# Optimization experiments

Hardware: AMD Instinct MI355X
Metric: run time of the kernel (lower is better)

Reference implementation:

```python
import jax, jax.numpy as jnp
import numpy as np


def lstm_encode(x, Wih, Whh, b):
    """x: [S, T, F] -> final hidden state [S, H]. PyTorch LSTM gate order (i, f, g, o)."""
    S = x.shape[0]
    H = Whh.shape[1]

    def step(carry, xt):
        h, c = carry
        z = xt @ Wih.T + h @ Whh.T + b  # [S, 4H]
        i, f, g, o = jnp.split(z, 4, axis=-1)
        c = jax.nn.sigmoid(f) * c + jax.nn.sigmoid(i) * jnp.tanh(g)
        h = jax.nn.sigmoid(o) * jnp.tanh(c)
        return (h, c), None

    init = (jnp.zeros((S, H), x.dtype), jnp.zeros((S, H), x.dtype))
    (h, _), _ = jax.lax.scan(step, init, jnp.swapaxes(x, 0, 1))
    return h


def gatv2(h, Ws, Wd, a, bias):
    """Dense GATv2 on batched fully-connected graphs (no self loops).
    h: [G, N, Hin]; Ws, Wd: [nh, Hin, O]; a: [nh, O]; bias: [nh, O] -> [G, N, nh, O].
    Graph is fully connected (all i != j), so edge-softmax == dense row softmax
    with the diagonal masked out; this is the efficient dense form of the
    gather / LeakyReLU / edge-softmax / scatter pattern in DGL's GATv2Conv."""
    nh = Ws.shape[0]
    N = h.shape[1]
    self_mask = jnp.eye(N, dtype=bool)
    outs = []
    for hd in range(nh):  # small fixed head count; loop caps peak memory
        fs = h @ Ws[hd]  # [G, N, O] source-projected feats (messages)
        fd = h @ Wd[hd]  # [G, N, O] dst-projected feats
        e = jax.nn.leaky_relu(fd[:, :, None, :] + fs[:, None, :, :], 0.2)  # [G, dst, src, O]
        logits = jnp.where(self_mask, -jnp.inf, e @ a[hd])  # [G, dst, src]
        attn = jax.nn.softmax(logits, axis=-1)
        outs.append(jnp.einsum('gds,gso->gdo', attn, fs) + bias[hd])
    return jnp.stack(outs, axis=2)


def cosine(x, y, eps=1e-6):
    xn = x / jnp.maximum(jnp.linalg.norm(x, axis=-1, keepdims=True), eps)
    yn = y / jnp.maximum(jnp.linalg.norm(y, axis=-1, keepdims=True), eps)
    return (xn * yn).sum(-1)


def setup_inputs() -> dict:
    key = jax.random.key(0)
    B, K, T, N, F, H, GH, NH = 16, 4, 64, 128, 16, 32, 32, 8
    ks = jax.random.split(key, 16)

    def rn(k, shape, scale=1.0):
        return jax.random.normal(k, shape, jnp.float32) * scale

    return {
        'anchor': rn(ks[0], (B, T, N, F)),
        'pos': rn(ks[1], (B, T, N, F)),
        'neg': rn(ks[2], (B, K, T, N, F)),
        'hideout': rn(ks[3], (B, 2)),
        'timestep': jax.random.uniform(ks[4], (B, 1), jnp.float32),
        'Wih': rn(ks[5], (4 * H, F), 1.0 / np.sqrt(F)),
        'Whh': rn(ks[6], (4 * H, H), 1.0 / np.sqrt(H)),
        'b_lstm': rn(ks[7], (4 * H,), 0.1),
        'W1s': rn(ks[8], (NH, H, H), 1.0 / np.sqrt(H)),
        'W1d': rn(ks[9], (NH, H, H), 1.0 / np.sqrt(H)),
        'a1': rn(ks[10], (NH, H), 1.0 / np.sqrt(H)),
        'b1': rn(ks[11], (NH, H), 0.1),
        'W2s': rn(ks[12], (1, H, GH), 1.0 / np.sqrt(H)),
        'W2d': rn(ks[13], (1, H, GH), 1.0 / np.sqrt(H)),
        'a2': rn(ks[14], (1, GH), 1.0 / np.sqrt(GH)),
        'b2': rn(ks[15], (1, GH), 0.1),
        'num_agents': 128,
    }


def reference(anchor, pos, neg, hideout, timestep, Wih, Whh, b_lstm,
              W1s, W1d, a1, b1, W2s, W2d, a2, b2, num_agents):
    B, T, N, F = anchor.shape
    K = neg.shape[1]
    H = Whh.shape[1]
    # per-agent time series -> LSTM sequences
    a_seq = jnp.transpose(anchor, (0, 2, 1, 3)).reshape(B * N, T, F)
    p_seq = jnp.transpose(pos, (0, 2, 1, 3)).reshape(B * N, T, F)
    n_seq = jnp.transpose(neg, (0, 1, 3, 2, 4)).reshape(B * K * N, T, F)
    hn = lstm_encode(jnp.concatenate([a_seq, p_seq, n_seq], 0), Wih, Whh, b_lstm)
    hg = hn.reshape(-1, N, H)  # [(2+K)*B, N, H] batched fully-connected graphs
    h1 = gatv2(hg, W1s, W1d, a1, b1).mean(axis=2)  # mean over 8 heads
    h2 = gatv2(h1, W2s, W2d, a2, b2)[:, :, 0, :]   # single head, squeezed
    pooled = h2.mean(axis=1)                        # AvgPooling over nodes
    anchor_res = pooled[:B]
    pos_res = pooled[B:2 * B]
    neg_res = pooled[2 * B:].reshape(B, K, -1)
    sim_pos = cosine(anchor_res, pos_res)[:, None]      # [B, 1]
    sim_neg = cosine(anchor_res[:, None, :], neg_res)   # [B, K]
    all_vecs = jnp.concatenate([sim_neg, sim_pos], axis=1)  # positive last
    contrastive = (-jax.nn.log_softmax(all_vecs, axis=1)[:, -1]).mean()
    res = jnp.concatenate([anchor_res, hideout, timestep], axis=-1)
    return res, contrastive
```

## Files before the change

### kernel.cpp

```cpp
#include <hip/hip_runtime.h>
#include <math.h>


typedef __bf16 bf16x8 __attribute__((ext_vector_type(8)));
typedef float  f32x4  __attribute__((ext_vector_type(4)));
typedef unsigned int u32x4 __attribute__((ext_vector_type(4)));

__device__ __forceinline__ float fast_rcp(float x) { return __builtin_amdgcn_rcpf(x); }
__device__ __forceinline__ float sigm(float x)     { return fast_rcp(1.f + __expf(-x)); }
__device__ __forceinline__ float tanh_fast(float x){ return fmaf(2.f, fast_rcp(1.f + __expf(-2.f * x)), -1.f); }

#define KEEP4(x) asm volatile("" : "+v"(x))

__global__ __launch_bounds__(256, 1) void lstm_mfma_kernel(
    const float* __restrict__ anchor, const float* __restrict__ pos,
    const float* __restrict__ neg, const float* __restrict__ Wih,
    const float* __restrict__ Whh, const float* __restrict__ bias,
    float* __restrict__ hn)
{
    __shared__ unsigned int Hbuf[4][512];
    const int tid  = threadIdx.x;
    const int w    = tid >> 6;
    const int lane = tid & 63;
    const int l15  = lane & 15;
    const int g4   = lane >> 4;
    unsigned int* hb = Hbuf[w];

    #pragma unroll
    for (int i = 0; i < 8; ++i) hb[lane + i * 64] = 0u;

    u32x4 whhH[8], whhL[8], wihH[8];
    float bq[8];
    #pragma unroll
    for (int f = 0; f < 8; ++f) {
        const int G = f >> 1, Hh = f & 1;
        const int c = G * 32 + Hh * 16 + l15;
        bq[f] = bias[c];
        union { u32x4 u; bf16x8 v; } th, tl, ti;
        const float* wr = Whh + c * 32 + g4 * 8;
        #pragma unroll
        for (int i = 0; i < 8; ++i) {
            float wv = wr[i];
            __bf16 hi = (__bf16)wv;
            th.v[i] = hi;
            tl.v[i] = (__bf16)(wv - (float)hi);
        }
        if (g4 < 2) {
            const float* wr2 = Wih + c * 16 + g4 * 8;
            #pragma unroll
            for (int i = 0; i < 8; ++i) ti.v[i] = (__bf16)wr2[i];
        } else {
            #pragma unroll
            for (int i = 0; i < 8; ++i) ti.v[i] = (__bf16)0.f;
        }
        whhH[f] = th.u; whhL[f] = tl.u; wihH[f] = ti.u;
    }
    #pragma unroll
    for (int f = 0; f < 8; ++f) { KEEP4(whhH[f]); KEEP4(whhL[f]); KEEP4(wihH[f]); }

    const int s = blockIdx.x * 64 + w * 16 + l15;
    const float* xbase; int sl;
    if (s < 2048)      { xbase = anchor; sl = s; }
    else if (s < 4096) { xbase = pos;    sl = s - 2048; }
    else               { xbase = neg;    sl = s - 4096; }
    const bool xact = (g4 < 2);
    const float* xp = xbase + (sl >> 7) * 131072 + (sl & 127) * 16 + (xact ? g4 * 8 : 0);

    const float4 z4 = make_float4(0.f, 0.f, 0.f, 0.f);
    float4 xaA = z4, xbA = z4, xaB = z4, xbB = z4;
    if (xact) {
        xaA = *(const float4*)(xp);        xbA = *(const float4*)(xp + 4);
        xaB = *(const float4*)(xp + 2048); xbB = *(const float4*)(xp + 2052);
    }

    float cst[8] = {0.f,0.f,0.f,0.f,0.f,0.f,0.f,0.f};
    float hv[8]  = {0.f,0.f,0.f,0.f,0.f,0.f,0.f,0.f};

    #define LSTM_STEP(XA, XB)                                                          \
    {                                                                                  \
        bf16x8 ax;                                                                     \
        ax[0]=(__bf16)XA.x; ax[1]=(__bf16)XA.y; ax[2]=(__bf16)XA.z; ax[3]=(__bf16)XA.w;\
        ax[4]=(__bf16)XB.x; ax[5]=(__bf16)XB.y; ax[6]=(__bf16)XB.z; ax[7]=(__bf16)XB.w;\
        const int c0 = g4 * 2;                                                         \
        const int swz = (l15 & 3) << 1;                                                \
        uint4 v0 = *(const uint4*)(hb + l15 * 32 + ((c0 ^ swz) << 2));                 \
        uint4 v1 = *(const uint4*)(hb + l15 * 32 + (((c0 + 1) ^ swz) << 2));           \
        union { unsigned int u[4]; bf16x8 v; } ahi, alo;                               \
        ahi.u[0] = __builtin_amdgcn_perm(v0.y, v0.x, 0x05040100u);                     \
        ahi.u[1] = __builtin_amdgcn_perm(v0.w, v0.z, 0x05040100u);                     \
        ahi.u[2] = __builtin_amdgcn_perm(v1.y, v1.x, 0x05040100u);                     \
        ahi.u[3] = __builtin_amdgcn_perm(v1.w, v1.z, 0x05040100u);                     \
        alo.u[0] = __builtin_amdgcn_perm(v0.y, v0.x, 0x07060302u);                     \
        alo.u[1] = __builtin_amdgcn_perm(v0.w, v0.z, 0x07060302u);                     \
        alo.u[2] = __builtin_amdgcn_perm(v1.y, v1.x, 0x07060302u);                     \
        alo.u[3] = __builtin_amdgcn_perm(v1.w, v1.z, 0x07060302u);                     \
        f32x4 z[8];                                                                    \
        _Pragma("unroll")                                                              \
        for (int f = 0; f < 8; ++f) {                                                  \
            f32x4 a = __builtin_amdgcn_mfma_f32_16x16x32_bf16(                         \
                ax, __builtin_bit_cast(bf16x8, wihH[f]), (f32x4)(0.f), 0, 0, 0);       \
            a = __builtin_amdgcn_mfma_f32_16x16x32_bf16(                               \
                ahi.v, __builtin_bit_cast(bf16x8, whhH[f]), a, 0, 0, 0);               \
            a = __builtin_amdgcn_mfma_f32_16x16x32_bf16(                               \
                ahi.v, __builtin_bit_cast(bf16x8, whhL[f]), a, 0, 0, 0);               \
            a = __builtin_amdgcn_mfma_f32_16x16x32_bf16(                               \
                alo.v, __builtin_bit_cast(bf16x8, whhH[f]), a, 0, 0, 0);               \
            z[f] = a;                                                                  \
        }                                                                              \
        _Pragma("unroll")                                                              \
        for (int Hh = 0; Hh < 2; ++Hh) {                                               \
            _Pragma("unroll")                                                          \
            for (int r = 0; r < 4; ++r) {                                              \
                const int idx = Hh * 4 + r;                                            \
                float zi = z[0 + Hh][r] + bq[0 + Hh];                                  \
                float zf = z[2 + Hh][r] + bq[2 + Hh];                                  \
                float zg = z[4 + Hh][r] + bq[4 + Hh];                                  \
                float zo = z[6 + Hh][r] + bq[6 + Hh];                                  \
                float cn = fmaf(sigm(zf), cst[idx], sigm(zi) * tanh_fast(zg));         \
                cst[idx] = cn;                                                         \
                float h = sigm(zo) * tanh_fast(cn);                                    \
                hv[idx] = h;                                                           \
                __bf16 hh_ = (__bf16)h;                                                \
                __bf16 hl_ = (__bf16)(h - (float)hh_);                                 \
                unsigned int pk = (unsigned int)__builtin_bit_cast(unsigned short, hh_)\
                                | ((unsigned int)__builtin_bit_cast(unsigned short, hl_) << 16); \
                const int mm = g4 * 4 + r;                                             \
                const int jw = Hh * 16 + l15;                                          \
                hb[mm * 32 + (((jw >> 2) ^ ((mm & 3) << 1)) << 2) + (jw & 3)] = pk;    \
            }                                                                          \
        }                                                                              \
    }

    for (int t = 0; t < 64; t += 2) {
        float4 cA1 = xaA, cA2 = xbA;
        if (xact && t + 2 < 64) {
            const float* p = xp + (t + 2) * 2048;
            xaA = *(const float4*)(p); xbA = *(const float4*)(p + 4);
        }
        LSTM_STEP(cA1, cA2);

        float4 cB1 = xaB, cB2 = xbB;
        if (xact && t + 3 < 64) {
            const float* p = xp + (t + 3) * 2048;
            xaB = *(const float4*)(p); xbB = *(const float4*)(p + 4);
        }
        LSTM_STEP(cB1, cB2);
    }
    #undef LSTM_STEP

    const int seq0 = blockIdx.x * 64 + w * 16;
    #pragma unroll
    for (int Hh = 0; Hh < 2; ++Hh) {
        #pragma unroll
        for (int r = 0; r < 4; ++r) {
            hn[(seq0 + g4 * 4 + r) * 32 + Hh * 16 + l15] = hv[Hh * 4 + r];
        }
    }
}

__global__ __launch_bounds__(256) void gat1_kernel(
    const float* __restrict__ hn, const float* __restrict__ W1s,
    const float* __restrict__ W1d, const float* __restrict__ a1,
    const float* __restrict__ b1, float* __restrict__ h1heads)
{
    const int g = blockIdx.x >> 3, hd = blockIdx.x & 7;
    __shared__ float FS[128][36];
    __shared__ float FD[128][36];
    __shared__ float AVr[32];
    __shared__ float As06[128];
    __shared__ float Ad06[128];
    const int tid = threadIdx.x;

    if (tid < 32) AVr[tid] = a1[hd * 32 + tid];

    {
        const int o = tid & 31, nb = tid >> 5;
        float wcs[32], wcd[32];
        const float* wsp = W1s + hd * 1024 + o;
        const float* wdp = W1d + hd * 1024 + o;
        #pragma unroll
        for (int k = 0; k < 32; ++k) { wcs[k] = wsp[k * 32]; wcd[k] = wdp[k * 32]; }
        const float* hp = hn + g * 4096 + nb * 512;
        #pragma unroll 1
        for (int n = 0; n < 16; ++n) {
            float a0 = 0.f, a1_ = 0.f, b0 = 0.f, b1_ = 0.f;
            #pragma unroll
            for (int k0 = 0; k0 < 32; k0 += 4) {
                float4 hv = *(const float4*)(hp + n * 32 + k0);
                a0 = fmaf(hv.x, wcs[k0+0], a0); b0 = fmaf(hv.x, wcd[k0+0], b0);
                a1_ = fmaf(hv.y, wcs[k0+1], a1_); b1_ = fmaf(hv.y, wcd[k0+1], b1_);
                a0 = fmaf(hv.z, wcs[k0+2], a0); b0 = fmaf(hv.z, wcd[k0+2], b0);
                a1_ = fmaf(hv.w, wcs[k0+3], a1_); b1_ = fmaf(hv.w, wcd[k0+3], b1_);
            }
            FS[nb * 16 + n][o] = a0 + a1_;
            FD[nb * 16 + n][o] = b0 + b1_;
        }
    }
    __syncthreads();

    if (tid < 128) {
        float ss = 0.f, sd = 0.f;
        #pragma unroll
        for (int oo = 0; oo < 32; ++oo) {
            int o = (oo + tid) & 31;
            float a = AVr[o];
            ss = fmaf(a, FS[tid][o], ss);
            sd = fmaf(a, FD[tid][o], sd);
        }
        As06[tid] = 0.6f * ss;
        Ad06[tid] = 0.6f * sd;
    }
    __syncthreads();

    const int d = tid >> 1, sbase = (tid & 1) << 6;
    float fdr[32], avs[32];
    #pragma unroll
    for (int c = 0; c < 8; ++c) {
        float4 v = *(const float4*)&FD[d][c * 4];
        fdr[c*4+0] = v.x; fdr[c*4+1] = v.y; fdr[c*4+2] = v.z; fdr[c*4+3] = v.w;
        float4 w = *(const float4*)&AVr[c * 4];
        avs[c*4+0] = 0.4f * w.x; avs[c*4+1] = 0.4f * w.y;
        avs[c*4+2] = 0.4f * w.z; avs[c*4+3] = 0.4f * w.w;
    }
    const float adc = Ad06[d];

    float Z = 0.f;
    float acc[32];
    #pragma unroll
    for (int o = 0; o < 32; ++o) acc[o] = 0.f;
    #pragma unroll 1
    for (int si = 0; si < 64; ++si) {
        const int s = sbase + si;
        float4 fa[8];
        #pragma unroll
        for (int c = 0; c < 8; ++c) fa[c] = *(const float4*)&FS[s][c * 4];
        float c0 = 0.f, c1 = 0.f, c2 = 0.f, c3 = 0.f;
        #pragma unroll
        for (int c = 0; c < 8; ++c) {
            float e0 = fdr[c*4+0] + fa[c].x; c0 = fmaf(avs[c*4+0], __builtin_fabsf(e0), c0);
            float e1 = fdr[c*4+1] + fa[c].y; c1 = fmaf(avs[c*4+1], __builtin_fabsf(e1), c1);
            float e2 = fdr[c*4+2] + fa[c].z; c2 = fmaf(avs[c*4+2], __builtin_fabsf(e2), c2);
            float e3 = fdr[c*4+3] + fa[c].w; c3 = fmaf(avs[c*4+3], __builtin_fabsf(e3), c3);
        }
        float v = adc + As06[s] + ((c0 + c1) + (c2 + c3));
        float e = (s == d) ? 0.f : __expf(v);
        Z += e;
        #pragma unroll
        for (int c = 0; c < 8; ++c) {
            acc[c*4+0] = fmaf(e, fa[c].x, acc[c*4+0]);
            acc[c*4+1] = fmaf(e, fa[c].y, acc[c*4+1]);
            acc[c*4+2] = fmaf(e, fa[c].z, acc[c*4+2]);
            acc[c*4+3] = fmaf(e, fa[c].w, acc[c*4+3]);
        }
    }
    Z += __shfl_xor(Z, 1);
    const float rz = fast_rcp(Z);
    #pragma unroll
    for (int o = 0; o < 32; ++o) acc[o] += __shfl_xor(acc[o], 1);

    float* dst = h1heads + ((size_t)((g * 8 + hd) * 128 + d)) * 32;
    const float* bp = b1 + hd * 32;
    if ((tid & 1) == 0) {
        #pragma unroll
        for (int c = 0; c < 4; ++c) {
            float4 v;
            v.x = fmaf(acc[c*4+0], rz, bp[c*4+0]);
            v.y = fmaf(acc[c*4+1], rz, bp[c*4+1]);
            v.z = fmaf(acc[c*4+2], rz, bp[c*4+2]);
            v.w = fmaf(acc[c*4+3], rz, bp[c*4+3]);
            *(float4*)(dst + c * 4) = v;
        }
    } else {
        #pragma unroll
        for (int c = 4; c < 8; ++c) {
            float4 v;
            v.x = fmaf(acc[c*4+0], rz, bp[c*4+0]);
            v.y = fmaf(acc[c*4+1], rz, bp[c*4+1]);
            v.z = fmaf(acc[c*4+2], rz, bp[c*4+2]);
            v.w = fmaf(acc[c*4+3], rz, bp[c*4+3]);
            *(float4*)(dst + c * 4) = v;
        }
    }
}

__global__ __launch_bounds__(256) void gat2_kernel(
    const float* __restrict__ h1heads, const float* __restrict__ W2s,
    const float* __restrict__ W2d, const float* __restrict__ a2,
    const float* __restrict__ b2, float* __restrict__ pooled)
{
    const int g = blockIdx.x;
    __shared__ float HS[128][36];
    __shared__ float FS[128][36];
    __shared__ float FD[128][36];
    __shared__ float AVr[32];
    __shared__ float As06[128];
    __shared__ float Ad06[128];
    const int tid = threadIdx.x;

    if (tid < 32) AVr[tid] = a2[tid];

    {
        #pragma unroll
        for (int i = 0; i < 4; ++i) {
            int idx4 = i * 256 + tid;
            float sx = 0.f, sy = 0.f, sz = 0.f, sw = 0.f;
            #pragma unroll
            for (int hdd = 0; hdd < 8; ++hdd) {
                const float4* src = (const float4*)(h1heads + (size_t)(g * 8 + hdd) * 4096);
                float4 v = src[idx4];
                sx += v.x; sy += v.y; sz += v.z; sw += v.w;
            }
            int n = idx4 >> 3, k0 = (idx4 & 7) * 4;
            float4 r; r.x = sx * 0.125f; r.y = sy * 0.125f; r.z = sz * 0.125f; r.w = sw * 0.125f;
            *(float4*)&HS[n][k0] = r;
        }
    }
    __syncthreads();

    {
        const int o = tid & 31, nb = tid >> 5;
        float wcs[32], wcd[32];
        const float* wsp = W2s + o;
        const float* wdp = W2d + o;
        #pragma unroll
        for (int k = 0; k < 32; ++k) { wcs[k] = wsp[k * 32]; wcd[k] = wdp[k * 32]; }
        #pragma unroll 1
        for (int n = nb * 16; n < nb * 16 + 16; ++n) {
            float a0 = 0.f, a1_ = 0.f, b0 = 0.f, b1_ = 0.f;
            #pragma unroll
            for (int k0 = 0; k0 < 32; k0 += 4) {
                const float4 hv = *(const float4*)&HS[n][k0];
                a0 = fmaf(hv.x, wcs[k0+0], a0); b0 = fmaf(hv.x, wcd[k0+0], b0);
                a1_ = fmaf(hv.y, wcs[k0+1], a1_); b1_ = fmaf(hv.y, wcd[k0+1], b1_);
                a0 = fmaf(hv.z, wcs[k0+2], a0); b0 = fmaf(hv.z, wcd[k0+2], b0);
                a1_ = fmaf(hv.w, wcs[k0+3], a1_); b1_ = fmaf(hv.w, wcd[k0+3], b1_);
            }
            FS[n][o] = a0 + a1_;
            FD[n][o] = b0 + b1_;
        }
    }
    __syncthreads();

    if (tid < 128) {
        float ss = 0.f, sd = 0.f;
        #pragma unroll
        for (int oo = 0; oo < 32; ++oo) {
            int o = (oo + tid) & 31;
            float a = AVr[o];
            ss = fmaf(a, FS[tid][o], ss);
            sd = fmaf(a, FD[tid][o], sd);
        }
        As06[tid] = 0.6f * ss;
        Ad06[tid] = 0.6f * sd;
    }
    __syncthreads();

    const int d = tid >> 1, sbase = (tid & 1) << 6;
    float fdr[32], avs[32];
    #pragma unroll
    for (int c = 0; c < 8; ++c) {
        float4 v = *(const float4*)&FD[d][c * 4];
        fdr[c*4+0] = v.x; fdr[c*4+1] = v.y; fdr[c*4+2] = v.z; fdr[c*4+3] = v.w;
        float4 w = *(const float4*)&AVr[c * 4];
        avs[c*4+0] = 0.4f * w.x; avs[c*4+1] = 0.4f * w.y;
        avs[c*4+2] = 0.4f * w.z; avs[c*4+3] = 0.4f * w.w;
    }
    const float adc = Ad06[d];

    float Z = 0.f;
    float acc[32];
    #pragma unroll
    for (int o = 0; o < 32; ++o) acc[o] = 0.f;
    #pragma unroll 1
    for (int si = 0; si < 64; ++si) {
        const int s = sbase + si;
        float4 fa[8];
        #pragma unroll
        for (int c = 0; c < 8; ++c) fa[c] = *(const float4*)&FS[s][c * 4];
        float c0 = 0.f, c1 = 0.f, c2 = 0.f, c3 = 0.f;
        #pragma unroll
        for (int c = 0; c < 8; ++c) {
            float e0 = fdr[c*4+0] + fa[c].x; c0 = fmaf(avs[c*4+0], __builtin_fabsf(e0), c0);
            float e1 = fdr[c*4+1] + fa[c].y; c1 = fmaf(avs[c*4+1], __builtin_fabsf(e1), c1);
            float e2 = fdr[c*4+2] + fa[c].z; c2 = fmaf(avs[c*4+2], __builtin_fabsf(e2), c2);
            float e3 = fdr[c*4+3] + fa[c].w; c3 = fmaf(avs[c*4+3], __builtin_fabsf(e3), c3);
        }
        float v = adc + As06[s] + ((c0 + c1) + (c2 + c3));
        float e = (s == d) ? 0.f : __expf(v);
        Z += e;
        #pragma unroll
        for (int c = 0; c < 8; ++c) {
            acc[c*4+0] = fmaf(e, fa[c].x, acc[c*4+0]);
            acc[c*4+1] = fmaf(e, fa[c].y, acc[c*4+1]);
            acc[c*4+2] = fmaf(e, fa[c].z, acc[c*4+2]);
            acc[c*4+3] = fmaf(e, fa[c].w, acc[c*4+3]);
        }
    }
    Z += __shfl_xor(Z, 1);
    const float rz = fast_rcp(Z);
    #pragma unroll
    for (int o = 0; o < 32; ++o) acc[o] += __shfl_xor(acc[o], 1);

    __syncthreads();
    if ((tid & 1) == 0) {
        #pragma unroll
        for (int c = 0; c < 4; ++c) {
            float4 v;
            v.x = acc[c*4+0] * rz; v.y = acc[c*4+1] * rz;
            v.z = acc[c*4+2] * rz; v.w = acc[c*4+3] * rz;
            *(float4*)&FD[d][c * 4] = v;
        }
    } else {
        #pragma unroll
        for (int c = 4; c < 8; ++c) {
            float4 v;
            v.x = acc[c*4+0] * rz; v.y = acc[c*4+1] * rz;
            v.z = acc[c*4+2] * rz; v.w = acc[c*4+3] * rz;
            *(float4*)&FD[d][c * 4] = v;
        }
    }
    __syncthreads();

    if (tid < 32) {
        float sp = 0.f;
        #pragma unroll 1
        for (int n = 0; n < 128; ++n) sp += FD[n][tid];
        pooled[g * 32 + tid] = fmaf(sp, 1.f / 128.f, b2[tid]);
    }
}

__global__ void final_kernel(const float* __restrict__ pooled,
                             const float* __restrict__ hideout,
                             const float* __restrict__ timestep,
                             float* __restrict__ out)
{
    const int b = threadIdx.x;
    __shared__ float lossArr[16];
    if (b < 16) {
        const float* A  = pooled + b * 32;
        const float* Pv = pooled + (16 + b) * 32;
        float av[32];
        float na = 0.f;
        #pragma unroll
        for (int i = 0; i < 32; ++i) { av[i] = A[i]; na += av[i] * av[i]; }
        float npv = 0.f, dp = 0.f;
        #pragma unroll
        for (int i = 0; i < 32; ++i) { float p = Pv[i]; npv += p * p; dp += av[i] * p; }
        const float eps = 1e-6f;
        const float ia = 1.f / fmaxf(sqrtf(na), eps);
        const float sp = dp * ia / fmaxf(sqrtf(npv), eps);
        float sn[4];
        #pragma unroll
        for (int k = 0; k < 4; ++k) {
            const float* Nv = pooled + (32 + b * 4 + k) * 32;
            float nn = 0.f, dn = 0.f;
            #pragma unroll
            for (int i = 0; i < 32; ++i) { float q = Nv[i]; nn += q * q; dn += av[i] * q; }
            sn[k] = dn * ia / fmaxf(sqrtf(nn), eps);
        }
        float m = sp;
        #pragma unroll
        for (int k = 0; k < 4; ++k) m = fmaxf(m, sn[k]);
        float Z = expf(sp - m);
        #pragma unroll
        for (int k = 0; k < 4; ++k) Z += expf(sn[k] - m);
        lossArr[b] = logf(Z) + m - sp;
        float* r = out + b * 35;
        #pragma unroll
        for (int i = 0; i < 32; ++i) r[i] = av[i];
        r[32] = hideout[b * 2];
        r[33] = hideout[b * 2 + 1];
        r[34] = timestep[b];
    }
    __syncthreads();
    if (b == 0) {
        float s = 0.f;
        #pragma unroll
        for (int i = 0; i < 16; ++i) s += lossArr[i];
        out[560] = s * (1.f / 16.f);
    }
}

extern "C" void kernel_launch(void* const* d_in, const int* in_sizes, int n_in,
                              void* d_out, int out_size, void* d_ws, size_t ws_size,
                              hipStream_t stream) {
    const float* anchor   = (const float*)d_in[0];
    const float* pos      = (const float*)d_in[1];
    const float* neg      = (const float*)d_in[2];
    const float* hideout  = (const float*)d_in[3];
    const float* timestep = (const float*)d_in[4];
    const float* Wih      = (const float*)d_in[5];
    const float* Whh      = (const float*)d_in[6];
    const float* b_lstm   = (const float*)d_in[7];
    const float* W1s      = (const float*)d_in[8];
    const float* W1d      = (const float*)d_in[9];
    const float* a1       = (const float*)d_in[10];
    const float* b1       = (const float*)d_in[11];
    const float* W2s      = (const float*)d_in[12];
    const float* W2d      = (const float*)d_in[13];
    const float* a2       = (const float*)d_in[14];
    const float* b2       = (const float*)d_in[15];
    float* out = (float*)d_out;

    char* ws = (char*)d_ws;
    float* hn      = (float*)(ws);
    float* h1heads = (float*)(ws + 1605632);
    float* pooled  = (float*)(ws + 14188544);

    hipLaunchKernelGGL(lstm_mfma_kernel, dim3(192), dim3(256), 0, stream,
                       anchor, pos, neg, Wih, Whh, b_lstm, hn);
    hipLaunchKernelGGL(gat1_kernel,  dim3(768),  dim3(256), 0, stream,
                       hn, W1s, W1d, a1, b1, h1heads);
    hipLaunchKernelGGL(gat2_kernel,  dim3(96),   dim3(256), 0, stream,
                       h1heads, W2s, W2d, a2, b2, pooled);
    hipLaunchKernelGGL(final_kernel, dim3(1),    dim3(64),  0, stream,
                       pooled, hideout, timestep, out);
}
```

Before: 177.7 us.

## Interleave two independent LSTM sequence tiles per wave and pad GAT FS rows

The LSTM kernel now has each wave process two 16-sequence tiles (A and B) together, interleaving their MFMA chains and activations. This hides the serial latency of the recurrent dependency chain, and the grid is halved from 192 to 96 blocks. In the GAT kernels the FS shared buffer gets an extra padding offset every 64 rows, so the two half-waves reading different source ranges land on different LDS banks. The cost is fewer blocks than the chip has compute units and higher register pressure in the LSTM kernel.

```diff
diff --git a/kernel.cpp b/kernel.cpp
--- a/kernel.cpp
+++ b/kernel.cpp
@@ -18,16 +18,17 @@
     const float* __restrict__ Whh, const float* __restrict__ bias,
     float* __restrict__ hn)
 {
-    __shared__ unsigned int Hbuf[4][512];
+    __shared__ unsigned int Hbuf[4][1024];
     const int tid  = threadIdx.x;
     const int w    = tid >> 6;
     const int lane = tid & 63;
     const int l15  = lane & 15;
     const int g4   = lane >> 4;
-    unsigned int* hb = Hbuf[w];
-
-    #pragma unroll
-    for (int i = 0; i < 8; ++i) hb[lane + i * 64] = 0u;
+    unsigned int* hbA = Hbuf[w];
+    unsigned int* hbB = Hbuf[w] + 512;
+
+    #pragma unroll
+    for (int i = 0; i < 16; ++i) Hbuf[w][lane + i * 64] = 0u;
 
     u32x4 whhH[8], whhL[8], wihH[8];
     float bq[8];
@@ -58,105 +59,152 @@
     #pragma unroll
     for (int f = 0; f < 8; ++f) { KEEP4(whhH[f]); KEEP4(whhL[f]); KEEP4(wihH[f]); }
 
-    const int s = blockIdx.x * 64 + w * 16 + l15;
-    const float* xbase; int sl;
-    if (s < 2048)      { xbase = anchor; sl = s; }
-    else if (s < 4096) { xbase = pos;    sl = s - 2048; }
-    else               { xbase = neg;    sl = s - 4096; }
     const bool xact = (g4 < 2);
-    const float* xp = xbase + (sl >> 7) * 131072 + (sl & 127) * 16 + (xact ? g4 * 8 : 0);
+    const float* xpA; const float* xpB;
+    {
+        const int sA = blockIdx.x * 128 + w * 32 + l15;
+        const int sB = sA + 16;
+        const float* base; int sl;
+        if (sA < 2048)      { base = anchor; sl = sA; }
+        else if (sA < 4096) { base = pos;    sl = sA - 2048; }
+        else                { base = neg;    sl = sA - 4096; }
+        xpA = base + (sl >> 7) * 131072 + (sl & 127) * 16 + (xact ? g4 * 8 : 0);
+        if (sB < 2048)      { base = anchor; sl = sB; }
+        else if (sB < 4096) { base = pos;    sl = sB - 2048; }
+        else                { base = neg;    sl = sB - 4096; }
+        xpB = base + (sl >> 7) * 131072 + (sl & 127) * 16 + (xact ? g4 * 8 : 0);
+    }
 
     const float4 z4 = make_float4(0.f, 0.f, 0.f, 0.f);
-    float4 xaA = z4, xbA = z4, xaB = z4, xbB = z4;
+    float4 eA0 = z4, eA1 = z4, oA0 = z4, oA1 = z4;
+    float4 eB0 = z4, eB1 = z4, oB0 = z4, oB1 = z4;
     if (xact) {
-        xaA = *(const float4*)(xp);        xbA = *(const float4*)(xp + 4);
-        xaB = *(const float4*)(xp + 2048); xbB = *(const float4*)(xp + 2052);
-    }
-
-    float cst[8] = {0.f,0.f,0.f,0.f,0.f,0.f,0.f,0.f};
-    float hv[8]  = {0.f,0.f,0.f,0.f,0.f,0.f,0.f,0.f};
-
-    #define LSTM_STEP(XA, XB)                                                          \
-    {                                                                                  \
-        bf16x8 ax;                                                                     \
-        ax[0]=(__bf16)XA.x; ax[1]=(__bf16)XA.y; ax[2]=(__bf16)XA.z; ax[3]=(__bf16)XA.w;\
-        ax[4]=(__bf16)XB.x; ax[5]=(__bf16)XB.y; ax[6]=(__bf16)XB.z; ax[7]=(__bf16)XB.w;\
-        const int c0 = g4 * 2;                                                         \
-        const int swz = (l15 & 3) << 1;                                                \
-        uint4 v0 = *(const uint4*)(hb + l15 * 32 + ((c0 ^ swz) << 2));                 \
-        uint4 v1 = *(const uint4*)(hb + l15 * 32 + (((c0 + 1) ^ swz) << 2));           \
-        union { unsigned int u[4]; bf16x8 v; } ahi, alo;                               \
-        ahi.u[0] = __builtin_amdgcn_perm(v0.y, v0.x, 0x05040100u);                     \
-        ahi.u[1] = __builtin_amdgcn_perm(v0.w, v0.z, 0x05040100u);                     \
-        ahi.u[2] = __builtin_amdgcn_perm(v1.y, v1.x, 0x05040100u);                     \
-        ahi.u[3] = __builtin_amdgcn_perm(v1.w, v1.z, 0x05040100u);                     \
-        alo.u[0] = __builtin_amdgcn_perm(v0.y, v0.x, 0x07060302u);                     \
-        alo.u[1] = __builtin_amdgcn_perm(v0.w, v0.z, 0x07060302u);                     \
-        alo.u[2] = __builtin_amdgcn_perm(v1.y, v1.x, 0x07060302u);                     \
-        alo.u[3] = __builtin_amdgcn_perm(v1.w, v1.z, 0x07060302u);                     \
-        f32x4 z[8];                                                                    \
-        _Pragma("unroll")                                                              \
-        for (int f = 0; f < 8; ++f) {                                                  \
-            f32x4 a = __builtin_amdgcn_mfma_f32_16x16x32_bf16(                         \
-                ax, __builtin_bit_cast(bf16x8, wihH[f]), (f32x4)(0.f), 0, 0, 0);       \
-            a = __builtin_amdgcn_mfma_f32_16x16x32_bf16(                               \
-                ahi.v, __builtin_bit_cast(bf16x8, whhH[f]), a, 0, 0, 0);               \
-            a = __builtin_amdgcn_mfma_f32_16x16x32_bf16(                               \
-                ahi.v, __builtin_bit_cast(bf16x8, whhL[f]), a, 0, 0, 0);               \
-            a = __builtin_amdgcn_mfma_f32_16x16x32_bf16(                               \
-                alo.v, __builtin_bit_cast(bf16x8, whhH[f]), a, 0, 0, 0);               \
-            z[f] = a;                                                                  \
-        }                                                                              \
+        eA0 = *(const float4*)(xpA);        eA1 = *(const float4*)(xpA + 4);
+        oA0 = *(const float4*)(xpA + 2048); oA1 = *(const float4*)(xpA + 2052);
+        eB0 = *(const float4*)(xpB);        eB1 = *(const float4*)(xpB + 4);
+        oB0 = *(const float4*)(xpB + 2048); oB1 = *(const float4*)(xpB + 2052);
+    }
+
+    float cstA[8] = {0,0,0,0,0,0,0,0}, hvA[8] = {0,0,0,0,0,0,0,0};
+    float cstB[8] = {0,0,0,0,0,0,0,0}, hvB[8] = {0,0,0,0,0,0,0,0};
+
+    const int c0  = g4 * 2;
+    const int swz = (l15 & 3) << 1;
+    const int ro0 = l15 * 32 + ((c0 ^ swz) << 2);
+    const int ro1 = l15 * 32 + (((c0 + 1) ^ swz) << 2);
+
+    #define CVT_AX(DST, X0, X1)                                                        \
+        bf16x8 DST;                                                                    \
+        DST[0]=(__bf16)X0.x; DST[1]=(__bf16)X0.y; DST[2]=(__bf16)X0.z; DST[3]=(__bf16)X0.w; \
+        DST[4]=(__bf16)X1.x; DST[5]=(__bf16)X1.y; DST[6]=(__bf16)X1.z; DST[7]=(__bf16)X1.w;
+
+    #define READ_H(HB, AHI, ALO)                                                       \
+        union { unsigned int u[4]; bf16x8 v; } AHI, ALO;                               \
+        {                                                                              \
+            uint4 v0 = *(const uint4*)(HB + ro0);                                      \
+            uint4 v1 = *(const uint4*)(HB + ro1);                                      \
+            AHI.u[0] = __builtin_amdgcn_perm(v0.y, v0.x, 0x05040100u);                 \
+            AHI.u[1] = __builtin_amdgcn_perm(v0.w, v0.z, 0x05040100u);                 \
+            AHI.u[2] = __builtin_amdgcn_perm(v1.y, v1.x, 0x05040100u);                 \
+            AHI.u[3] = __builtin_amdgcn_perm(v1.w, v1.z, 0x05040100u);                 \
+            ALO.u[0] = __builtin_amdgcn_perm(v0.y, v0.x, 0x07060302u);                 \
+            ALO.u[1] = __builtin_amdgcn_perm(v0.w, v0.z, 0x07060302u);                 \
+            ALO.u[2] = __builtin_amdgcn_perm(v1.y, v1.x, 0x07060302u);                 \
+            ALO.u[3] = __builtin_amdgcn_perm(v1.w, v1.z, 0x07060302u);                 \
+        }
+
+    #define ACT_WRITE(Z, CST, HV, HB)                                                  \
         _Pragma("unroll")                                                              \
         for (int Hh = 0; Hh < 2; ++Hh) {                                               \
             _Pragma("unroll")                                                          \
             for (int r = 0; r < 4; ++r) {                                              \
                 const int idx = Hh * 4 + r;                                            \
-                float zi = z[0 + Hh][r] + bq[0 + Hh];                                  \
-                float zf = z[2 + Hh][r] + bq[2 + Hh];                                  \
-                float zg = z[4 + Hh][r] + bq[4 + Hh];                                  \
-                float zo = z[6 + Hh][r] + bq[6 + Hh];                                  \
-                float cn = fmaf(sigm(zf), cst[idx], sigm(zi) * tanh_fast(zg));         \
-                cst[idx] = cn;                                                         \
+                float zi = Z[0 + Hh][r] + bq[0 + Hh];                                  \
+                float zf = Z[2 + Hh][r] + bq[2 + Hh];                                  \
+                float zg = Z[4 + Hh][r] + bq[4 + Hh];                                  \
+                float zo = Z[6 + Hh][r] + bq[6 + Hh];                                  \
+                float cn = fmaf(sigm(zf), CST[idx], sigm(zi) * tanh_fast(zg));         \
+                CST[idx] = cn;                                                         \
                 float h = sigm(zo) * tanh_fast(cn);                                    \
-                hv[idx] = h;                                                           \
+                HV[idx] = h;                                                           \
                 __bf16 hh_ = (__bf16)h;                                                \
                 __bf16 hl_ = (__bf16)(h - (float)hh_);                                 \
                 unsigned int pk = (unsigned int)__builtin_bit_cast(unsigned short, hh_)\
                                 | ((unsigned int)__builtin_bit_cast(unsigned short, hl_) << 16); \
                 const int mm = g4 * 4 + r;                                             \
                 const int jw = Hh * 16 + l15;                                          \
-                hb[mm * 32 + (((jw >> 2) ^ ((mm & 3) << 1)) << 2) + (jw & 3)] = pk;    \
+                HB[mm * 32 + (((jw >> 2) ^ ((mm & 3) << 1)) << 2) + (jw & 3)] = pk;    \
             }                                                                          \
+        }
+
+    #define DUAL_STEP(XA0, XA1, XB0, XB1)                                              \
+    {                                                                                  \
+        READ_H(hbA, ahiA, aloA)                                                        \
+        READ_H(hbB, ahiB, aloB)                                                        \
+        CVT_AX(axA, XA0, XA1)                                                          \
+        CVT_AX(axB, XB0, XB1)                                                          \
+        f32x4 zA[8], zB[8];                                                            \
+        _Pragma("unroll")                                                              \
+        for (int f = 0; f < 8; ++f) {                                                  \
+            f32x4 a = __builtin_amdgcn_mfma_f32_16x16x32_bf16(                         \
+                axA, __builtin_bit_cast(bf16x8, wihH[f]), (f32x4)(0.f), 0, 0, 0);      \
+            a = __builtin_amdgcn_mfma_f32_16x16x32_bf16(                               \
+                ahiA.v, __builtin_bit_cast(bf16x8, whhH[f]), a, 0, 0, 0);              \
+            a = __builtin_amdgcn_mfma_f32_16x16x32_bf16(                               \
+                ahiA.v, __builtin_bit_cast(bf16x8, whhL[f]), a, 0, 0, 0);              \
+            a = __builtin_amdgcn_mfma_f32_16x16x32_bf16(                               \
+                aloA.v, __builtin_bit_cast(bf16x8, whhH[f]), a, 0, 0, 0);              \
+            zA[f] = a;                                                                 \
+            f32x4 b = __builtin_amdgcn_mfma_f32_16x16x32_bf16(                         \
+                axB, __builtin_bit_cast(bf16x8, wihH[f]), (f32x4)(0.f), 0, 0, 0);      \
+            b = __builtin_amdgcn_mfma_f32_16x16x32_bf16(                               \
+                ahiB.v, __builtin_bit_cast(bf16x8, whhH[f]), b, 0, 0, 0);              \
+            b = __builtin_amdgcn_mfma_f32_16x16x32_bf16(                               \
+                ahiB.v, __builtin_bit_cast(bf16x8, whhL[f]), b, 0, 0, 0);              \
+            b = __builtin_amdgcn_mfma_f32_16x16x32_bf16(                               \
+                aloB.v, __builtin_bit_cast(bf16x8, whhH[f]), b, 0, 0, 0);              \
+            zB[f] = b;                                                                 \
         }                                                                              \
+        ACT_WRITE(zA, cstA, hvA, hbA)                                                  \
+        ACT_WRITE(zB, cstB, hvB, hbB)                                                  \
     }
 
     for (int t = 0; t < 64; t += 2) {
-        float4 cA1 = xaA, cA2 = xbA;
+        float4 cA0 = eA0, cA1 = eA1, cB0 = eB0, cB1 = eB1;
         if (xact && t + 2 < 64) {
-            const float* p = xp + (t + 2) * 2048;
-            xaA = *(const float4*)(p); xbA = *(const float4*)(p + 4);
-        }
-        LSTM_STEP(cA1, cA2);
-
-        float4 cB1 = xaB, cB2 = xbB;
+            const float* pA = xpA + (t + 2) * 2048;
+            const float* pB = xpB + (t + 2) * 2048;
+            eA0 = *(const float4*)(pA); eA1 = *(const float4*)(pA + 4);
+            eB0 = *(const float4*)(pB); eB1 = *(const float4*)(pB + 4);
+        }
+        DUAL_STEP(cA0, cA1, cB0, cB1);
+
+        float4 dA0 = oA0, dA1 = oA1, dB0 = oB0, dB1 = oB1;
         if (xact && t + 3 < 64) {
-            const float* p = xp + (t + 3) * 2048;
-            xaB = *(const float4*)(p); xbB = *(const float4*)(p + 4);
-        }
-        LSTM_STEP(cB1, cB2);
-    }
-    #undef LSTM_STEP
-
-    const int seq0 = blockIdx.x * 64 + w * 16;
+            const float* pA = xpA + (t + 3) * 2048;
+            const float* pB = xpB + (t + 3) * 2048;
+            oA0 = *(const float4*)(pA); oA1 = *(const float4*)(pA + 4);
+            oB0 = *(const float4*)(pB); oB1 = *(const float4*)(pB + 4);
+        }
+        DUAL_STEP(dA0, dA1, dB0, dB1);
+    }
+    #undef DUAL_STEP
+    #undef ACT_WRITE
+    #undef READ_H
+    #undef CVT_AX
+
+    const int baseA = blockIdx.x * 128 + w * 32;
     #pragma unroll
     for (int Hh = 0; Hh < 2; ++Hh) {
         #pragma unroll
         for (int r = 0; r < 4; ++r) {
-            hn[(seq0 + g4 * 4 + r) * 32 + Hh * 16 + l15] = hv[Hh * 4 + r];
+            hn[(baseA + g4 * 4 + r) * 32 + Hh * 16 + l15]      = hvA[Hh * 4 + r];
+            hn[(baseA + 16 + g4 * 4 + r) * 32 + Hh * 16 + l15] = hvB[Hh * 4 + r];
         }
     }
 }
+
+__device__ __forceinline__ int fsoff(int n) { return n * 36 + ((n >> 6) << 2); }
 
 __global__ __launch_bounds__(256) void gat1_kernel(
     const float* __restrict__ hn, const float* __restrict__ W1s,
@@ -164,7 +212,7 @@
     const float* __restrict__ b1, float* __restrict__ h1heads)
 {
     const int g = blockIdx.x >> 3, hd = blockIdx.x & 7;
-    __shared__ float FS[128][36];
+    __shared__ float FSf[128 * 36 + 4];
     __shared__ float FD[128][36];
     __shared__ float AVr[32];
     __shared__ float As06[128];
@@ -192,19 +240,21 @@
                 a0 = fmaf(hv.z, wcs[k0+2], a0); b0 = fmaf(hv.z, wcd[k0+2], b0);
                 a1_ = fmaf(hv.w, wcs[k0+3], a1_); b1_ = fmaf(hv.w, wcd[k0+3], b1_);
             }
-            FS[nb * 16 + n][o] = a0 + a1_;
-            FD[nb * 16 + n][o] = b0 + b1_;
+            const int row = nb * 16 + n;
+            FSf[fsoff(row) + o] = a0 + a1_;
+            FD[row][o] = b0 + b1_;
         }
     }
     __syncthreads();
 
     if (tid < 128) {
         float ss = 0.f, sd = 0.f;
+        const float* fr = FSf + fsoff(tid);
         #pragma unroll
         for (int oo = 0; oo < 32; ++oo) {
             int o = (oo + tid) & 31;
             float a = AVr[o];
-            ss = fmaf(a, FS[tid][o], ss);
+            ss = fmaf(a, fr[o], ss);
             sd = fmaf(a, FD[tid][o], sd);
         }
         As06[tid] = 0.6f * ss;
@@ -231,9 +281,10 @@
     #pragma unroll 1
     for (int si = 0; si < 64; ++si) {
         const int s = sbase + si;
+        const float* fr = FSf + fsoff(s);
         float4 fa[8];
         #pragma unroll
-        for (int c = 0; c < 8; ++c) fa[c] = *(const float4*)&FS[s][c * 4];
+        for (int c = 0; c < 8; ++c) fa[c] = *(const float4*)(fr + c * 4);
         float c0 = 0.f, c1 = 0.f, c2 = 0.f, c3 = 0.f;
         #pragma unroll
         for (int c = 0; c < 8; ++c) {
@@ -290,7 +341,7 @@
 {
     const int g = blockIdx.x;
     __shared__ float HS[128][36];
-    __shared__ float FS[128][36];
+    __shared__ float FSf[128 * 36 + 4];
     __shared__ float FD[128][36];
     __shared__ float AVr[32];
     __shared__ float As06[128];
@@ -335,7 +386,7 @@
                 a0 = fmaf(hv.z, wcs[k0+2], a0); b0 = fmaf(hv.z, wcd[k0+2], b0);
                 a1_ = fmaf(hv.w, wcs[k0+3], a1_); b1_ = fmaf(hv.w, wcd[k0+3], b1_);
             }
-            FS[n][o] = a0 + a1_;
+            FSf[fsoff(n) + o] = a0 + a1_;
             FD[n][o] = b0 + b1_;
         }
     }
@@ -343,11 +394,12 @@
 
     if (tid < 128) {
         float ss = 0.f, sd = 0.f;
+        const float* fr = FSf + fsoff(tid);
         #pragma unroll
         for (int oo = 0; oo < 32; ++oo) {
             int o = (oo + tid) & 31;
             float a = AVr[o];
-            ss = fmaf(a, FS[tid][o], ss);
+            ss = fmaf(a, fr[o], ss);
             sd = fmaf(a, FD[tid][o], sd);
         }
         As06[tid] = 0.6f * ss;
@@ -374,9 +426,10 @@
     #pragma unroll 1
     for (int si = 0; si < 64; ++si) {
         const int s = sbase + si;
+        const float* fr = FSf + fsoff(s);
         float4 fa[8];
         #pragma unroll
-        for (int c = 0; c < 8; ++c) fa[c] = *(const float4*)&FS[s][c * 4];
+        for (int c = 0; c < 8; ++c) fa[c] = *(const float4*)(fr + c * 4);
         float c0 = 0.f, c1 = 0.f, c2 = 0.f, c3 = 0.f;
         #pragma unroll
         for (int c = 0; c < 8; ++c) {
@@ -507,7 +560,7 @@
     float* h1heads = (float*)(ws + 1605632);
     float* pooled  = (float*)(ws + 14188544);
 
-    hipLaunchKernelGGL(lstm_mfma_kernel, dim3(192), dim3(256), 0, stream,
+    hipLaunchKernelGGL(lstm_mfma_kernel, dim3(96), dim3(256), 0, stream,
                        anchor, pos, neg, Wih, Whh, b_lstm, hn);
     hipLaunchKernelGGL(gat1_kernel,  dim3(768),  dim3(256), 0, stream,
                        hn, W1s, W1d, a1, b1, h1heads);
```

Result: slower. 234.0 us (+31.7%).
